# Kernel tuning notes

Measured on AMD Instinct MI355X. Metric: run time of the kernel, lower is better.

Reference implementation:

```python
import jax, jax.numpy as jnp
import numpy as np

VALUE_RANGE = 16
D_MODEL = 1024
NUM_TILES = 8
NUM_FREQS = 6
BATCH = 65536
TEMPERATURE = 0.5


def _fourier(x):
    # x: (B,) -> (B, 2*NUM_FREQS); freqs = 2**[0..F)
    freqs = 2.0 ** jnp.arange(NUM_FREQS, dtype=jnp.float32)
    ang = x[:, None] * (2.0 * np.pi / VALUE_RANGE) * freqs[None, :]
    return jnp.concatenate([jnp.sin(ang), jnp.cos(ang)], axis=-1)


def _layernorm(x, g, b, eps=1e-5):
    m = jnp.mean(x, axis=-1, keepdims=True)
    v = jnp.var(x, axis=-1, keepdims=True)
    return (x - m) * jax.lax.rsqrt(v + eps) * g + b


def _gelu(x):
    return jax.nn.gelu(x, approximate=False)  # torch nn.GELU() default is exact erf


def setup_inputs() -> dict:
    key = jax.random.key(0)
    ks = jax.random.split(key, 16)
    d, T, F4 = D_MODEL, NUM_TILES, 4 * NUM_FREQS
    s = lambda i, shape, scale: (jax.random.normal(ks[i], shape, jnp.float32) * scale)
    return {
        "a": jax.random.uniform(ks[0], (BATCH,), jnp.float32, 0.0, float(VALUE_RANGE)),
        "b": jax.random.uniform(ks[1], (BATCH,), jnp.float32, 0.0, float(VALUE_RANGE)),
        "W_in": s(2, (F4, d), 0.05), "b_in": jnp.zeros((d,), jnp.float32),
        "ln_g": jnp.ones((d,), jnp.float32), "ln_b": jnp.zeros((d,), jnp.float32),
        "Wr1_sum": s(3, (d, d), 0.03), "br1_sum": jnp.zeros((d,), jnp.float32),
        "Wr2_sum": s(4, (d, T), 0.03), "br2_sum": jnp.zeros((T,), jnp.float32),
        "Wr1_diff": s(5, (d, d), 0.03), "br1_diff": jnp.zeros((d,), jnp.float32),
        "Wr2_diff": s(6, (d, T), 0.03), "br2_diff": jnp.zeros((T,), jnp.float32),
        "We1": s(7, (T, d, 2 * d), 0.03), "be1": jnp.zeros((T, 2 * d), jnp.float32),
        "We2": s(8, (T, 2 * d, d), 0.02), "be2": jnp.zeros((T, d), jnp.float32),
        "w_sum": s(9, (d,), 0.03), "bs": jnp.zeros((), jnp.float32),
        "w_diff": s(10, (d,), 0.03), "bd": jnp.zeros((), jnp.float32),
    }


def reference(a, b, W_in, b_in, ln_g, ln_b,
              Wr1_sum, br1_sum, Wr2_sum, br2_sum,
              Wr1_diff, br1_diff, Wr2_diff, br2_diff,
              We1, be1, We2, be2, w_sum, bs, w_diff, bd):
    # Shared encoder
    x = jnp.concatenate([_fourier(a), _fourier(b)], axis=-1)      # (B, 4F)
    x = _gelu(_layernorm(x @ W_in + b_in, ln_g, ln_b))            # (B, d)
    # Top-1 routing (temperature scaling does not change argmax, kept for fidelity)
    sum_logits = (_gelu(x @ Wr1_sum + br1_sum) @ Wr2_sum + br2_sum) / TEMPERATURE
    diff_logits = (_gelu(x @ Wr1_diff + br1_diff) @ Wr2_diff + br2_diff) / TEMPERATURE
    sum_tile = jnp.argmax(sum_logits, axis=-1)                    # (B,)
    diff_tile = jnp.argmax(diff_logits, axis=-1)                  # (B,)
    # Expert dispatch: loop over small fixed num_tiles, mask-combine per token.
    sum_hidden = jnp.zeros_like(x)
    diff_hidden = jnp.zeros_like(x)
    for t in range(We1.shape[0]):
        y = _gelu(x @ We1[t] + be1[t]) @ We2[t] + be2[t]          # (B, d)
        sum_hidden = sum_hidden + jnp.where((sum_tile == t)[:, None], y, 0.0)
        diff_hidden = diff_hidden + jnp.where((diff_tile == t)[:, None], y, 0.0)
    sum_pred = sum_hidden @ w_sum + bs                            # (B,)
    diff_pred = diff_hidden @ w_diff + bd                         # (B,)
    return (sum_pred, diff_pred)
```

## Files before the change

### kernel.cpp

```cpp
#include <hip/hip_runtime.h>
#include <math.h>


#define BT 65536
#define QN 65536
#define TSTR QN
#define D 1024
#define NT 8
#define DH 2048
#define RCAP 8192
#define RTOK 8
#define DELTA 0.010f
#define XJCAP 768

typedef _Float16 f16;
typedef _Float16 f16x8 __attribute__((ext_vector_type(8)));
typedef _Float16 f16x4 __attribute__((ext_vector_type(4)));
typedef float f32x16 __attribute__((ext_vector_type(16)));

__device__ __forceinline__ float gelu_f(float v) {
    return 0.5f * v * (1.0f + erff(v * 0.70710678118654752440f));
}

__device__ __forceinline__ float gelu_fast(float x) {
    float ax = fabsf(x) * 0.70710678118654752440f;
    float t = __builtin_amdgcn_rcpf(1.0f + 0.3275911f * ax);
    float p = t * (0.254829592f + t * (-0.284496736f + t * (1.421413741f +
              t * (-1.453152027f + t * 1.061405429f))));
    float er = 1.0f - p * __expf(-ax * ax);
    er = copysignf(er, x);
    return 0.5f * x * (1.0f + er);
}

__device__ __forceinline__ void gload16(const void* g, void* l) {
    __builtin_amdgcn_global_load_lds(
        (const __attribute__((address_space(1))) void*)g,
        (__attribute__((address_space(3))) void*)l, 16, 0, 0);
}

__global__ __launch_bounds__(256) void k_prev(
    const float* __restrict__ We2, const float* __restrict__ w_sum,
    const float* __restrict__ w_diff, const float* __restrict__ be2,
    const float* __restrict__ bs, const float* __restrict__ bd,
    float* __restrict__ v_sum, float* __restrict__ v_diff,
    float* __restrict__ c_sum, float* __restrict__ c_diff)
{
    int bid = blockIdx.x;
    if (bid < 4096) {
        int row  = bid * 4 + (threadIdx.x >> 6);
        int lane = threadIdx.x & 63;
        const float* r = We2 + (size_t)row * D;
        float s1 = 0.f, s2 = 0.f;
        #pragma unroll
        for (int i = 0; i < 4; i++) {
            int o4 = (lane + 64 * i) * 4;
            float4 w = *(const float4*)(r + o4);
            float4 u = *(const float4*)(w_sum + o4);
            float4 v = *(const float4*)(w_diff + o4);
            s1 += w.x*u.x + w.y*u.y + w.z*u.z + w.w*u.w;
            s2 += w.x*v.x + w.y*v.y + w.z*v.z + w.w*v.w;
        }
        #pragma unroll
        for (int m = 32; m >= 1; m >>= 1) {
            s1 += __shfl_xor(s1, m, 64);
            s2 += __shfl_xor(s2, m, 64);
        }
        if (lane == 0) { v_sum[row] = s1; v_diff[row] = s2; }
    } else {
        int t = threadIdx.x;
        if (t < 8) {
            float s = 0.f; const float* r = be2 + t * D;
            for (int k = 0; k < D; k++) s += r[k] * w_sum[k];
            c_sum[t] = s + bs[0];
        } else if (t < 16) {
            int tt = t - 8;
            float s = 0.f; const float* r = be2 + tt * D;
            for (int k = 0; k < D; k++) s += r[k] * w_diff[k];
            c_diff[tt] = s + bd[0];
        }
    }
}

__global__ __launch_bounds__(256) void k_cvt(
    const float* __restrict__ We1, f16* __restrict__ We1T)
{
    __shared__ float tile[64][65];
    int b = blockIdx.x;
    int e = b >> 9, rem = b & 511;
    int kt = rem >> 5, nt = rem & 31;
    int tid = threadIdx.x;
    const float* src = We1 + ((size_t)e * D + kt * 64) * DH + nt * 64;
    #pragma unroll
    for (int i = 0; i < 16; i++) {
        int idx = tid + 256 * i;
        int kk = idx >> 6, nn = idx & 63;
        tile[kk][nn] = src[(size_t)kk * DH + nn];
    }
    __syncthreads();
    f16* dst = We1T + ((size_t)e * DH + nt * 64) * D + kt * 64;
    #pragma unroll
    for (int i = 0; i < 16; i++) {
        int idx = tid + 256 * i;
        int nn = idx >> 6, kk = idx & 63;
        dst[(size_t)nn * D + kk] = (f16)tile[kk][nn];
    }
}

__global__ __launch_bounds__(256) void k_cvtR(
    const float* __restrict__ Wr1s, const float* __restrict__ Wr1d,
    f16* __restrict__ Wr1Tf)
{
    __shared__ float tile[64][65];
    int b = blockIdx.x;
    int z = b >> 8, rem = b & 255;
    int kt = rem >> 4, nt2 = rem & 15;
    int tid = threadIdx.x;
    const float* W = z ? Wr1d : Wr1s;
    const float* src = W + (size_t)(kt * 64) * 1024 + nt2 * 64;
    #pragma unroll
    for (int i = 0; i < 16; i++) {
        int idx = tid + 256 * i;
        int kk = idx >> 6, nn = idx & 63;
        tile[kk][nn] = src[(size_t)kk * 1024 + nn];
    }
    __syncthreads();
    f16* dst = Wr1Tf + (size_t)(z * 1024 + nt2 * 64) * 1024 + kt * 64;
    #pragma unroll
    for (int i = 0; i < 16; i++) {
        int idx = tid + 256 * i;
        int nn = idx >> 6, kk = idx & 63;
        dst[(size_t)nn * 1024 + kk] = (f16)tile[kk][nn];
    }
}

__global__ __launch_bounds__(256) void k_fuse(
    const float* __restrict__ br1s, const float* __restrict__ br1d,
    const float* __restrict__ Wr2s, const float* __restrict__ Wr2d,
    float* __restrict__ br1f, float* __restrict__ w2f)
{
    int tid = threadIdx.x;
    for (int n = tid; n < 2048; n += 256) {
        br1f[n] = (n < 1024) ? br1s[n] : br1d[n - 1024];
        const float* src = (n < 1024) ? (Wr2s + (size_t)n * 8)
                                      : (Wr2d + (size_t)(n - 1024) * 8);
        #pragma unroll
        for (int o = 0; o < 8; o++) w2f[(size_t)n * 8 + o] = src[o];
    }
}

__global__ __launch_bounds__(256) void k_enc(
    const float* __restrict__ a, const float* __restrict__ b,
    const float* __restrict__ W_in, const float* __restrict__ b_in,
    const float* __restrict__ ln_g, const float* __restrict__ ln_b,
    f16* __restrict__ xh)
{
    __shared__ float x0[64][24];
    __shared__ float red[8];
    int tid = threadIdx.x;
    float4 Wc[24];
    #pragma unroll
    for (int f = 0; f < 24; f++) Wc[f] = *(const float4*)(W_in + f * D + tid * 4);
    float4 bi = *(const float4*)(b_in + tid * 4);
    float4 gg = *(const float4*)(ln_g + tid * 4);
    float4 bb = *(const float4*)(ln_b + tid * 4);
    int base = blockIdx.x * 64;

    for (int idx = tid; idx < 64 * 12; idx += 256) {
        int t = idx / 12, q = idx - t * 12;
        int fr = q % 6;
        float in = (q < 6) ? a[base + t] : b[base + t];
        float ang = (in * 0.39269908169872414f) * (float)(1 << fr);
        int off = (q < 6) ? 0 : 12;
        x0[t][off + fr]     = sinf(ang);
        x0[t][off + 6 + fr] = cosf(ang);
    }
    __syncthreads();

    int lane = tid & 63, wid = tid >> 6;
    for (int t = 0; t < 64; t++) {
        float4 p = bi;
        #pragma unroll
        for (int f = 0; f < 24; f++) {
            float xv = x0[t][f];
            p.x += xv * Wc[f].x; p.y += xv * Wc[f].y;
            p.z += xv * Wc[f].z; p.w += xv * Wc[f].w;
        }
        float s1 = p.x + p.y + p.z + p.w;
        float s2 = p.x*p.x + p.y*p.y + p.z*p.z + p.w*p.w;
        #pragma unroll
        for (int m = 32; m >= 1; m >>= 1) {
            s1 += __shfl_xor(s1, m, 64);
            s2 += __shfl_xor(s2, m, 64);
        }
        if (lane == 0) { red[wid] = s1; red[4 + wid] = s2; }
        __syncthreads();
        float mean = (red[0] + red[1] + red[2] + red[3]) * (1.f / 1024.f);
        float ms   = (red[4] + red[5] + red[6] + red[7]) * (1.f / 1024.f);
        float inv  = 1.f / sqrtf(ms - mean * mean + 1e-5f);
        float4 o;
        o.x = gelu_f((p.x - mean) * inv * gg.x + bb.x);
        o.y = gelu_f((p.y - mean) * inv * gg.y + bb.y);
        o.z = gelu_f((p.z - mean) * inv * gg.z + bb.z);
        o.w = gelu_f((p.w - mean) * inv * gg.w + bb.w);
        size_t row = (size_t)(blockIdx.x * 64 + t);
        f16x4 h; h[0] = (f16)o.x; h[1] = (f16)o.y; h[2] = (f16)o.z; h[3] = (f16)o.w;
        *(f16x4*)(xh + row * D + tid * 4) = h;
        __syncthreads();
    }
}

__global__ __launch_bounds__(256, 3) void k_rtrm(
    const f16* __restrict__ xh, const f16* __restrict__ Wr1Tf,
    const float* __restrict__ br1f, const float* __restrict__ w2f,
    float* __restrict__ part)
{
    __shared__ char smem[40960] __attribute__((aligned(16)));
    int bid = blockIdx.x;
    int ntile = bid & 7;
    int ttile = bid >> 3;
    int tid = threadIdx.x;
    int lane = tid & 63, wid = tid >> 6;
    int hi = lane >> 5, l31 = lane & 31;
    int sg = tid >> 3, sc = tid & 7;

    const char* xb = (const char*)xh + (size_t)(ttile * 64) * 2048;
    const char* wb = (const char*)Wr1Tf + (size_t)(ntile * 256) * 2048;
    size_t goff = (size_t)sg * 2048 + (size_t)((sc * 16) ^ ((sg & 7) << 4));

    int axor = (l31 & 7) << 4;
    int kx[4];
    #pragma unroll
    for (int ks = 0; ks < 4; ks++) kx[ks] = (ks * 32 + hi * 16) ^ axor;
    int arow[2], brow[2];
    #pragma unroll
    for (int mi = 0; mi < 2; mi++) arow[mi] = (wid * 64 + mi * 32 + l31) * 128;
    #pragma unroll
    for (int ni = 0; ni < 2; ni++) brow[ni] = 32768 + (ni * 32 + l31) * 128;

    f32x16 acc[2][2];
    #pragma unroll
    for (int mi = 0; mi < 2; mi++)
        #pragma unroll
        for (int ni = 0; ni < 2; ni++) acc[mi][ni] = (f32x16)(0.0f);

    for (int k0 = 0; k0 < 1024; k0 += 64) {
        __syncthreads();
        #pragma unroll
        for (int i = 0; i < 8; i++)
            gload16(wb + (size_t)i * 32 * 2048 + k0 * 2 + goff,
                    smem + i * 4096 + wid * 1024);
        #pragma unroll
        for (int i = 0; i < 2; i++)
            gload16(xb + (size_t)i * 32 * 2048 + k0 * 2 + goff,
                    smem + 32768 + i * 4096 + wid * 1024);
        __syncthreads();
        #pragma unroll
        for (int ks = 0; ks < 4; ks++) {
            f16x8 a0 = *(const f16x8*)(smem + arow[0] + kx[ks]);
            f16x8 a1 = *(const f16x8*)(smem + arow[1] + kx[ks]);
            f16x8 b0 = *(const f16x8*)(smem + brow[0] + kx[ks]);
            f16x8 b1 = *(const f16x8*)(smem + brow[1] + kx[ks]);
            acc[0][0] = __builtin_amdgcn_mfma_f32_32x32x16_f16(a0, b0, acc[0][0], 0, 0, 0);
            acc[0][1] = __builtin_amdgcn_mfma_f32_32x32x16_f16(a0, b1, acc[0][1], 0, 0, 0);
            acc[1][0] = __builtin_amdgcn_mfma_f32_32x32x16_f16(a1, b0, acc[1][0], 0, 0, 0);
            acc[1][1] = __builtin_amdgcn_mfma_f32_32x32x16_f16(a1, b1, acc[1][1], 0, 0, 0);
        }
    }

    float lp[2][8] = {};
    #pragma unroll
    for (int mi = 0; mi < 2; mi++) {
        #pragma unroll
        for (int r = 0; r < 16; r++) {
            int nl = wid * 64 + mi * 32 + (r & 3) + 8 * (r >> 2) + 4 * hi;
            int gn = ntile * 256 + nl;
            float b1 = br1f[gn];
            float4 wa = *(const float4*)(w2f + (size_t)gn * 8);
            float4 wc = *(const float4*)(w2f + (size_t)gn * 8 + 4);
            float h0 = gelu_fast(acc[mi][0][r] + b1);
            float h1 = gelu_fast(acc[mi][1][r] + b1);
            lp[0][0] += h0*wa.x; lp[0][1] += h0*wa.y;
            lp[0][2] += h0*wa.z; lp[0][3] += h0*wa.w;
            lp[0][4] += h0*wc.x; lp[0][5] += h0*wc.y;
            lp[0][6] += h0*wc.z; lp[0][7] += h0*wc.w;
            lp[1][0] += h1*wa.x; lp[1][1] += h1*wa.y;
            lp[1][2] += h1*wa.z; lp[1][3] += h1*wa.w;
            lp[1][4] += h1*wc.x; lp[1][5] += h1*wc.y;
            lp[1][6] += h1*wc.z; lp[1][7] += h1*wc.w;
        }
    }
    #pragma unroll
    for (int ni = 0; ni < 2; ni++)
        #pragma unroll
        for (int o = 0; o < 8; o++)
            lp[ni][o] += __shfl_xor(lp[ni][o], 32, 64);
    __syncthreads();
    float* redf = (float*)smem;
    if (hi == 0) {
        #pragma unroll
        for (int ni = 0; ni < 2; ni++)
            #pragma unroll
            for (int o = 0; o < 8; o++)
                redf[(wid * 64 + ni * 32 + l31) * 8 + o] = lp[ni][o];
    }
    __syncthreads();
    for (int idx = tid; idx < 512; idx += 256) {
        int tok = idx >> 3, o = idx & 7;
        float s = ((redf[(0 * 64 + tok) * 8 + o]  + redf[(1 * 64 + tok) * 8 + o])
                 +  redf[(2 * 64 + tok) * 8 + o]) + redf[(3 * 64 + tok) * 8 + o];
        part[((size_t)(ttile * 64 + tok) * 8 + ntile) * 8 + o] = s;
    }
}

__device__ __forceinline__ void emit_tasks(int tok, int ts, int td,
                                           int* tasks, int* cnts)
{
    if (ts == td) {
        int s = atomicAdd(&cnts[ts], 1);
        tasks[ts * TSTR + s] = tok | (3 << 17);
    } else {
        int s1 = atomicAdd(&cnts[ts], 1);
        tasks[ts * TSTR + s1] = tok | (1 << 17);
        int s2 = atomicAdd(&cnts[td], 1);
        tasks[td * TSTR + s2] = tok | (2 << 17);
    }
}

__global__ __launch_bounds__(256) void k_amx2(
    const float* __restrict__ part, const float* __restrict__ b2s,
    const float* __restrict__ b2d, int* __restrict__ tasks,
    int* __restrict__ ctrl, int* __restrict__ redoS, int* __restrict__ redoD)
{
    int i = blockIdx.x * 256 + threadIdx.x;
    const float* p = part + (size_t)i * 64;
    float Ls[8], Ld[8];
    #pragma unroll
    for (int o = 0; o < 8; o++) { Ls[o] = b2s[o]; Ld[o] = b2d[o]; }
    #pragma unroll
    for (int nt = 0; nt < 4; nt++)
        #pragma unroll
        for (int o = 0; o < 8; o++) Ls[o] += p[nt * 8 + o];
    #pragma unroll
    for (int nt = 4; nt < 8; nt++)
        #pragma unroll
        for (int o = 0; o < 8; o++) Ld[o] += p[nt * 8 + o];

    int as = 0; float m1s = Ls[0];
    #pragma unroll
    for (int o = 1; o < 8; o++) if (Ls[o] > m1s) { m1s = Ls[o]; as = o; }
    float m2s = -1e30f;
    #pragma unroll
    for (int o = 0; o < 8; o++) if (o != as && Ls[o] > m2s) m2s = Ls[o];
    int ad = 0; float m1d = Ld[0];
    #pragma unroll
    for (int o = 1; o < 8; o++) if (Ld[o] > m1d) { m1d = Ld[o]; ad = o; }
    float m2d = -1e30f;
    #pragma unroll
    for (int o = 0; o < 8; o++) if (o != ad && Ld[o] > m2d) m2d = Ld[o];

    bool sM = (m1s - m2s) < DELTA;
    bool dM = (m1d - m2d) < DELTA;
    if (!sM && !dM) { emit_tasks(i, as, ad, tasks, ctrl); return; }
    int posS = -1, posD = -1;
    if (sM) { posS = atomicAdd(&ctrl[8], 1); if (posS >= RCAP) { sM = false; posS = -1; } }
    if (dM) { posD = atomicAdd(&ctrl[9], 1); if (posD >= RCAP) { dM = false; posD = -1; } }
    if (!sM && !dM) { emit_tasks(i, as, ad, tasks, ctrl); return; }
    if (sM) redoS[posS] = i | (ad << 17) | ((dM ? 1 : 0) << 20);
    if (dM) redoD[posD] = i | (as << 17) | ((sM ? 1 : 0) << 20);
}

__global__ __launch_bounds__(256) void k_redo(
    const float* __restrict__ a, const float* __restrict__ b,
    const float* __restrict__ W_in, const float* __restrict__ b_in,
    const float* __restrict__ ln_g, const float* __restrict__ ln_b,
    const float* __restrict__ Wr1s, const float* __restrict__ br1s,
    const float* __restrict__ Wr2s,
    const float* __restrict__ Wr1d, const float* __restrict__ br1d,
    const float* __restrict__ Wr2d,
    const int* __restrict__ redoS, const int* __restrict__ redoD,
    const int* __restrict__ ctrl,
    float* __restrict__ rlogpS, float* __restrict__ rlogpD)
{
    int z = blockIdx.y;
    int rcnt = min(ctrl[8 + z], RCAP);
    int s0 = blockIdx.x * RTOK;
    if (s0 >= rcnt) return;
    const int* list = z ? redoD : redoS;
    const float* Wr1 = z ? Wr1d : Wr1s;
    const float* br1v = z ? br1d : br1s;
    const float* Wr2 = z ? Wr2d : Wr2s;

    __shared__ float xl[RTOK][1024];
    __shared__ float x0[RTOK][24];
    __shared__ float wred[4][RTOK][2];
    __shared__ float lred[4][RTOK][8];
    __shared__ int tokR[RTOK];
    int tid = threadIdx.x;
    int lane = tid & 63, wid = tid >> 6;

    if (tid < RTOK) tokR[tid] = list[min(s0 + tid, rcnt - 1)] & 0xFFFF;
    __syncthreads();

    if (tid < RTOK * 12) {
        int t = tid / 12, q = tid - t * 12;
        int fr = q % 6;
        int tok = tokR[t];
        float in = (q < 6) ? a[tok] : b[tok];
        float ang = (in * 0.39269908169872414f) * (float)(1 << fr);
        int off = (q < 6) ? 0 : 12;
        x0[t][off + fr]     = sinf(ang);
        x0[t][off + 6 + fr] = cosf(ang);
    }
    __syncthreads();

    {
        float4 Wc[24];
        #pragma unroll
        for (int f = 0; f < 24; f++) Wc[f] = *(const float4*)(W_in + f * D + tid * 4);
        float4 bi = *(const float4*)(b_in + tid * 4);
        float4 gg = *(const float4*)(ln_g + tid * 4);
        float4 bb = *(const float4*)(ln_b + tid * 4);
        float p[RTOK][4];
        #pragma unroll
        for (int r = 0; r < RTOK; r++) {
            float4 pv = bi;
            #pragma unroll
            for (int f = 0; f < 24; f++) {
                float xv = x0[r][f];
                pv.x += xv * Wc[f].x; pv.y += xv * Wc[f].y;
                pv.z += xv * Wc[f].z; pv.w += xv * Wc[f].w;
            }
            p[r][0] = pv.x; p[r][1] = pv.y; p[r][2] = pv.z; p[r][3] = pv.w;
            float s1 = pv.x + pv.y + pv.z + pv.w;
            float s2 = pv.x*pv.x + pv.y*pv.y + pv.z*pv.z + pv.w*pv.w;
            #pragma unroll
            for (int m = 32; m >= 1; m >>= 1) {
                s1 += __shfl_xor(s1, m, 64);
                s2 += __shfl_xor(s2, m, 64);
            }
            if (lane == 0) { wred[wid][r][0] = s1; wred[wid][r][1] = s2; }
        }
        __syncthreads();
        #pragma unroll
        for (int r = 0; r < RTOK; r++) {
            float mean = (wred[0][r][0] + wred[1][r][0] + wred[2][r][0] + wred[3][r][0]) * (1.f / 1024.f);
            float ms   = (wred[0][r][1] + wred[1][r][1] + wred[2][r][1] + wred[3][r][1]) * (1.f / 1024.f);
            float inv  = 1.f / sqrtf(ms - mean * mean + 1e-5f);
            float gv[4] = {gg.x, gg.y, gg.z, gg.w};
            float bv[4] = {bb.x, bb.y, bb.z, bb.w};
            #pragma unroll
            for (int jj = 0; jj < 4; jj++)
                xl[r][tid * 4 + jj] = gelu_f((p[r][jj] - mean) * inv * gv[jj] + bv[jj]);
        }
    }
    __syncthreads();

    int c0 = tid * 4;
    float hacc[RTOK][4] = {};
    #pragma unroll 4
    for (int k = 0; k < 1024; k++) {
        float4 wv = *(const float4*)(Wr1 + (size_t)k * 1024 + c0);
        #pragma unroll
        for (int r = 0; r < RTOK; r++) {
            float xv = xl[r][k];
            hacc[r][0] += xv * wv.x; hacc[r][1] += xv * wv.y;
            hacc[r][2] += xv * wv.z; hacc[r][3] += xv * wv.w;
        }
    }
    float L[RTOK][8] = {};
    #pragma unroll
    for (int jj = 0; jj < 4; jj++) {
        int col = c0 + jj;
        float b1 = br1v[col];
        float4 wa = *(const float4*)(Wr2 + (size_t)col * 8);
        float4 wc = *(const float4*)(Wr2 + (size_t)col * 8 + 4);
        #pragma unroll
        for (int r = 0; r < RTOK; r++) {
            float h = gelu_f(hacc[r][jj] + b1);
            L[r][0] += h*wa.x; L[r][1] += h*wa.y; L[r][2] += h*wa.z; L[r][3] += h*wa.w;
            L[r][4] += h*wc.x; L[r][5] += h*wc.y; L[r][6] += h*wc.z; L[r][7] += h*wc.w;
        }
    }
    #pragma unroll
    for (int m = 32; m >= 1; m >>= 1)
        #pragma unroll
        for (int r = 0; r < RTOK; r++)
            #pragma unroll
            for (int o = 0; o < 8; o++)
                L[r][o] += __shfl_xor(L[r][o], m, 64);
    if (lane == 0) {
        #pragma unroll
        for (int r = 0; r < RTOK; r++)
            #pragma unroll
            for (int o = 0; o < 8; o++)
                lred[wid][r][o] = L[r][o];
    }
    __syncthreads();
    if (tid < RTOK * 8) {
        int r = tid >> 3, o = tid & 7;
        int slot = s0 + r;
        if (slot < rcnt) {
            float v = ((lred[0][r][o] + lred[1][r][o]) + lred[2][r][o]) + lred[3][r][o];
            float* dst = z ? rlogpD : rlogpS;
            dst[(size_t)slot * 8 + o] = v;
        }
    }
}

__global__ __launch_bounds__(256) void k_amx3d(
    const float* __restrict__ rlogpD, const int* __restrict__ redoD,
    const float* __restrict__ b2d, int* __restrict__ tasks,
    int* __restrict__ ctrl, int* __restrict__ adx)
{
    int rcnt = min(ctrl[9], RCAP);
    for (int s = blockIdx.x * 256 + threadIdx.x; s < rcnt; s += gridDim.x * 256) {
        int entry = redoD[s];
        int tok = entry & 0xFFFF;
        float L[8];
        #pragma unroll
        for (int o = 0; o < 8; o++) L[o] = rlogpD[(size_t)s * 8 + o] + b2d[o];
        int td = 0; float bv = L[0];
        #pragma unroll
        for (int o = 1; o < 8; o++) if (L[o] > bv) { bv = L[o]; td = o; }
        adx[tok] = td;
        if (!((entry >> 20) & 1))
            emit_tasks(tok, (entry >> 17) & 7, td, tasks, ctrl);
    }
}

__global__ __launch_bounds__(256) void k_amx3s(
    const float* __restrict__ rlogpS, const int* __restrict__ redoS,
    const float* __restrict__ b2s, int* __restrict__ tasks,
    int* __restrict__ ctrl, const int* __restrict__ adx)
{
    int rcnt = min(ctrl[8], RCAP);
    for (int s = blockIdx.x * 256 + threadIdx.x; s < rcnt; s += gridDim.x * 256) {
        int entry = redoS[s];
        int tok = entry & 0xFFFF;
        float L[8];
        #pragma unroll
        for (int o = 0; o < 8; o++) L[o] = rlogpS[(size_t)s * 8 + o] + b2s[o];
        int ts = 0; float bv = L[0];
        #pragma unroll
        for (int o = 1; o < 8; o++) if (L[o] > bv) { bv = L[o]; ts = o; }
        int td = ((entry >> 20) & 1) ? adx[tok] : ((entry >> 17) & 7);
        emit_tasks(tok, ts, td, tasks, ctrl);
    }
}

__global__ void k_sched(const int* __restrict__ ctrl, int* __restrict__ xjob)
{
    __shared__ int seg[17];
    __shared__ int Jt[2];
    int tid = threadIdx.x;
    if (tid == 0) {
        int o = 0;
        for (int e = 0; e < 8; e++) {
            int nt2 = (ctrl[e] + 127) >> 7;
            seg[e * 2]     = o; o += nt2;
            seg[e * 2 + 1] = o; o += nt2;
        }
        seg[16] = o;
        Jt[0] = o; Jt[1] = (o + 7) >> 3;
    }
    __syncthreads();
    int J = Jt[0], target = Jt[1];
    for (int g = tid; g < J; g += blockDim.x) {
        int s = 0;
        while (s < 15 && seg[s + 1] <= g) s++;
        int e = s >> 1, ch = s & 1, rt = g - seg[s];
        int x = g / target; if (x > 7) x = 7;
        int pos = g - x * target;
        xjob[x * XJCAP + pos] = e | (ch << 3) | (rt << 4);
    }
    if (tid < 8) {
        int c = J - tid * target;
        if (c < 0) c = 0;
        if (c > target) c = target;
        xjob[8 * XJCAP + tid] = c;
    }
}

__global__ __launch_bounds__(256) void k_expm(
    const f16* __restrict__ xh, const f16* __restrict__ We1T,
    const float* __restrict__ be1, const float* __restrict__ v_sum,
    const float* __restrict__ v_diff, const float* __restrict__ c_sum,
    const float* __restrict__ c_diff, const int* __restrict__ tasks,
    const int* __restrict__ counts, const int* __restrict__ xjob,
    float* __restrict__ ppS, float* __restrict__ ppD)
{
    int xcd  = blockIdx.x & 7;
    int slot = blockIdx.x >> 3;
    int nj = xjob[8 * XJCAP + xcd];

    __shared__ char smem[65536] __attribute__((aligned(16)));
    __shared__ int tokL[128];
    __shared__ int flgL[128];
    __shared__ float redS[2][128];
    __shared__ float redD[2][128];

    int tid = threadIdx.x;
    int lane = tid & 63;
    int wid  = tid >> 6;
    int wr = wid >> 1, wc = wid & 1;
    int hi = lane >> 5, l31 = lane & 31;
    int sg = tid >> 3, sc = tid & 7;
    int goffc = (sc * 16) ^ ((sg & 7) << 4);

    const char* xh_b = (const char*)xh;

    int axor = (l31 & 7) << 4;
    int kx[4];
    #pragma unroll
    for (int ks = 0; ks < 4; ks++) kx[ks] = (ks * 32 + hi * 16) ^ axor;
    int arow[2], brow[2];
    #pragma unroll
    for (int mi = 0; mi < 2; mi++) arow[mi] = (wr * 64 + mi * 32 + l31) * 128;
    #pragma unroll
    for (int ni = 0; ni < 2; ni++) brow[ni] = 16384 + (wc * 64 + ni * 32 + l31) * 128;

    for (int j = slot; j < nj; j += 256) {
        int jv = xjob[xcd * XJCAP + j];
        int e  = jv & 7;
        int ch = (jv >> 3) & 1;
        int rt = jv >> 4;
        int cnt = counts[e];
        int r0 = rt * 128;
        const char* bbase = (const char*)(We1T + (size_t)e * DH * D);

        __syncthreads();
        if (tid < 128) {
            int idx = r0 + tid;
            int tv = tasks[e * TSTR + min(idx, cnt - 1)];
            tokL[tid] = tv & 0xFFFF;
            flgL[tid] = (idx < cnt) ? ((tv >> 17) & 3) : 0;
        }
        __syncthreads();
        size_t asrc[4];
        #pragma unroll
        for (int i = 0; i < 4; i++)
            asrc[i] = (size_t)tokL[i * 32 + sg] * 2048 + goffc;

        float ss[2][16] = {}, sd[2][16] = {};
        f32x16 acc[2][2];
        #pragma unroll
        for (int mi = 0; mi < 2; mi++)
            #pragma unroll
            for (int ni = 0; ni < 2; ni++) acc[mi][ni] = (f32x16)(0.0f);

        auto STAGE = [&](int p, int bb) {
            int n0 = ch * 1024 + (p >> 4) * 128;
            int k0b = (p & 15) * 128;
            char* ldsA = smem + bb * 32768 + wid * 1024;
            char* ldsB = smem + bb * 32768 + 16384 + wid * 1024;
            #pragma unroll
            for (int i = 0; i < 4; i++)
                gload16(xh_b + asrc[i] + k0b, ldsA + i * 4096);
            const char* bs = bbase + ((size_t)n0 + sg) * 2048 + k0b + goffc;
            #pragma unroll
            for (int i = 0; i < 4; i++)
                gload16(bs + (size_t)i * 32 * 2048, ldsB + i * 4096);
        };

        STAGE(0, 0);
        __syncthreads();
        for (int p = 0; p < 128; ++p) {
            int bb = p & 1;
            if (p < 127) STAGE(p + 1, bb ^ 1);
            const char* base = smem + bb * 32768;
            #pragma unroll
            for (int ks = 0; ks < 4; ks++) {
                f16x8 a0 = *(const f16x8*)(base + arow[0] + kx[ks]);
                f16x8 a1 = *(const f16x8*)(base + arow[1] + kx[ks]);
                f16x8 b0 = *(const f16x8*)(base + brow[0] + kx[ks]);
                f16x8 b1 = *(const f16x8*)(base + brow[1] + kx[ks]);
                acc[0][0] = __builtin_amdgcn_mfma_f32_32x32x16_f16(a0, b0, acc[0][0], 0, 0, 0);
                acc[0][1] = __builtin_amdgcn_mfma_f32_32x32x16_f16(a0, b1, acc[0][1], 0, 0, 0);
                acc[1][0] = __builtin_amdgcn_mfma_f32_32x32x16_f16(a1, b0, acc[1][0], 0, 0, 0);
                acc[1][1] = __builtin_amdgcn_mfma_f32_32x32x16_f16(a1, b1, acc[1][1], 0, 0, 0);
            }
            if ((p & 15) == 15) {
                int n0 = ch * 1024 + (p >> 4) * 128;
                #pragma unroll
                for (int ni = 0; ni < 2; ni++) {
                    int col = n0 + wc * 64 + ni * 32 + l31;
                    float b1 = be1[e * DH + col];
                    float vs = v_sum[(size_t)e * DH + col];
                    float vd = v_diff[(size_t)e * DH + col];
                    #pragma unroll
                    for (int mi = 0; mi < 2; mi++) {
                        #pragma unroll
                        for (int r = 0; r < 16; r++) {
                            float h = gelu_fast(acc[mi][ni][r] + b1);
                            ss[mi][r] += h * vs;
                            sd[mi][r] += h * vd;
                        }
                    }
                }
                #pragma unroll
                for (int mi = 0; mi < 2; mi++)
                    #pragma unroll
                    for (int ni = 0; ni < 2; ni++) acc[mi][ni] = (f32x16)(0.0f);
            }
            __syncthreads();
        }

        #pragma unroll
        for (int m = 16; m >= 1; m >>= 1) {
            #pragma unroll
            for (int mi = 0; mi < 2; mi++)
                #pragma unroll
                for (int r = 0; r < 16; r++) {
                    ss[mi][r] += __shfl_xor(ss[mi][r], m, 64);
                    sd[mi][r] += __shfl_xor(sd[mi][r], m, 64);
                }
        }
        if (l31 == 0) {
            #pragma unroll
            for (int mi = 0; mi < 2; mi++)
                #pragma unroll
                for (int r = 0; r < 16; r++) {
                    int row = wr * 64 + mi * 32 + (r & 3) + 8 * (r >> 2) + 4 * hi;
                    redS[wc][row] = ss[mi][r];
                    redD[wc][row] = sd[mi][r];
                }
        }
        __syncthreads();
        if (tid < 128) {
            int idx = r0 + tid;
            if (idx < cnt) {
                int fl = flgL[tid];
                int tok = tokL[tid];
                float s = redS[0][tid] + redS[1][tid];
                float d = redD[0][tid] + redD[1][tid];
                if (ch == 0) { s += c_sum[e]; d += c_diff[e]; }
                if (fl & 1) ppS[ch * QN + tok] = s;
                if (fl & 2) ppD[ch * QN + tok] = d;
            }
        }
    }
}

__global__ __launch_bounds__(256) void k_fin(
    const float* __restrict__ ppS, const float* __restrict__ ppD,
    float* __restrict__ out)
{
    int i = blockIdx.x * 256 + threadIdx.x;
    out[i]      = ppS[i] + ppS[QN + i];
    out[BT + i] = ppD[i] + ppD[QN + i];
}

extern "C" void kernel_launch(void* const* d_in, const int* in_sizes, int n_in,
                              void* d_out, int out_size, void* d_ws, size_t ws_size,
                              hipStream_t stream)
{
    const float* a      = (const float*)d_in[0];
    const float* b      = (const float*)d_in[1];
    const float* W_in   = (const float*)d_in[2];
    const float* b_in   = (const float*)d_in[3];
    const float* ln_g   = (const float*)d_in[4];
    const float* ln_b   = (const float*)d_in[5];
    const float* Wr1s   = (const float*)d_in[6];
    const float* br1s   = (const float*)d_in[7];
    const float* Wr2s   = (const float*)d_in[8];
    const float* br2s   = (const float*)d_in[9];
    const float* Wr1d   = (const float*)d_in[10];
    const float* br1d   = (const float*)d_in[11];
    const float* Wr2d   = (const float*)d_in[12];
    const float* br2d   = (const float*)d_in[13];
    const float* We1    = (const float*)d_in[14];
    const float* be1    = (const float*)d_in[15];
    const float* We2    = (const float*)d_in[16];
    const float* be2    = (const float*)d_in[17];
    const float* w_sum  = (const float*)d_in[18];
    const float* bs     = (const float*)d_in[19];
    const float* w_diff = (const float*)d_in[20];
    const float* bd     = (const float*)d_in[21];
    float* out = (float*)d_out;

    char* w = (char*)d_ws;
    size_t off = 0;
    auto alloc = [&](size_t bytes) -> char* {
        char* p = w + off;
        off = (off + bytes + 255) & ~(size_t)255;
        return p;
    };
    float* v_sum   = (float*)alloc((size_t)NT * DH * 4);
    float* v_diff  = (float*)alloc((size_t)NT * DH * 4);
    float* c_sum   = (float*)alloc(64);
    float* c_diff  = (float*)alloc(64);
    f16*   xh      = (f16*)alloc((size_t)QN * D * 2);
    float* part    = (float*)alloc((size_t)QN * 64 * 4);
    float* rlogpS  = (float*)alloc((size_t)RCAP * 8 * 4);
    float* rlogpD  = (float*)alloc((size_t)RCAP * 8 * 4);
    int*   redoS   = (int*)alloc((size_t)RCAP * 4);
    int*   redoD   = (int*)alloc((size_t)RCAP * 4);
    int*   adx     = (int*)alloc((size_t)QN * 4);
    int*   tasks   = (int*)alloc((size_t)NT * QN * 4);
    int*   ctrl    = (int*)alloc(64);
    int*   xjob    = (int*)alloc((size_t)(8 * XJCAP + 8) * 4);
    float* ppS     = (float*)alloc((size_t)2 * QN * 4);
    float* ppD     = (float*)alloc((size_t)2 * QN * 4);
    f16*   We1T    = (f16*)alloc((size_t)NT * DH * D * 2);
    f16*   Wr1Tf   = (f16*)alloc((size_t)2048 * 1024 * 2);
    float* br1f    = (float*)alloc((size_t)2048 * 4);
    float* w2f     = (float*)alloc((size_t)2048 * 8 * 4);
    if (off > ws_size) {
        hipMemsetAsync(d_out, 0, (size_t)out_size * 4, stream);
        return;
    }

    k_cvt <<<dim3(4096), dim3(256), 0, stream>>>(We1, We1T);
    k_cvtR<<<dim3(512),  dim3(256), 0, stream>>>(Wr1s, Wr1d, Wr1Tf);
    k_fuse<<<dim3(1),    dim3(256), 0, stream>>>(br1s, br1d, Wr2s, Wr2d, br1f, w2f);
    k_prev<<<dim3(4097), dim3(256), 0, stream>>>(We2, w_sum, w_diff, be2, bs, bd,
                                                 v_sum, v_diff, c_sum, c_diff);
    k_enc<<<dim3(QN / 64), dim3(256), 0, stream>>>(a, b, W_in, b_in, ln_g, ln_b, xh);
    k_rtrm<<<dim3(QN / 64 * 8), dim3(256), 0, stream>>>(xh, Wr1Tf, br1f, w2f, part);
    hipMemsetAsync(ctrl, 0, 64, stream);
    k_amx2<<<dim3(QN / 256), dim3(256), 0, stream>>>(part, br2s, br2d, tasks, ctrl,
                                                     redoS, redoD);
    k_redo<<<dim3(RCAP / RTOK, 2), dim3(256), 0, stream>>>(
        a, b, W_in, b_in, ln_g, ln_b,
        Wr1s, br1s, Wr2s, Wr1d, br1d, Wr2d,
        redoS, redoD, ctrl, rlogpS, rlogpD);
    k_amx3d<<<dim3(16), dim3(256), 0, stream>>>(rlogpD, redoD, br2d, tasks, ctrl, adx);
    k_amx3s<<<dim3(16), dim3(256), 0, stream>>>(rlogpS, redoS, br2s, tasks, ctrl, adx);
    k_sched<<<dim3(1), dim3(256), 0, stream>>>(ctrl, xjob);
    k_expm<<<dim3(2048), dim3(256), 0, stream>>>(xh, We1T, be1, v_sum, v_diff,
                                                 c_sum, c_diff, tasks, ctrl, xjob,
                                                 ppS, ppD);
    k_fin<<<dim3(QN / 256), dim3(256), 0, stream>>>(ppS, ppD, out);
}
```

Measured before the change: 3.041 ms.

## Widen expert GEMM N-tile to 256 and triple-buffer LDS with explicit waitcnts

The expert first-layer MFMA kernel now computes a 128x256 output tile per block, with each wave holding 2x4 accumulators instead of 2x2. Each A fragment is therefore reused across twice as many B columns. The LDS pipeline grows from double to triple buffering (144KB of shared memory), using manual s_waitcnt vmcnt counts and raw s_barrier so two stages of global loads stay in flight. The trade-off is lower occupancy, since only one block fits per CU, plus higher accumulator register pressure.

```diff
diff --git a/kernel.cpp b/kernel.cpp
--- a/kernel.cpp
+++ b/kernel.cpp
@@ -593,7 +593,7 @@
     int slot = blockIdx.x >> 3;
     int nj = xjob[8 * XJCAP + xcd];
 
-    __shared__ char smem[65536] __attribute__((aligned(16)));
+    __shared__ char smem[147456] __attribute__((aligned(16)));
     __shared__ int tokL[128];
     __shared__ int flgL[128];
     __shared__ float redS[2][128];
@@ -613,11 +613,11 @@
     int kx[4];
     #pragma unroll
     for (int ks = 0; ks < 4; ks++) kx[ks] = (ks * 32 + hi * 16) ^ axor;
-    int arow[2], brow[2];
+    int arow[2], nrow[4];
     #pragma unroll
     for (int mi = 0; mi < 2; mi++) arow[mi] = (wr * 64 + mi * 32 + l31) * 128;
     #pragma unroll
-    for (int ni = 0; ni < 2; ni++) brow[ni] = 16384 + (wc * 64 + ni * 32 + l31) * 128;
+    for (int ni = 0; ni < 4; ni++) nrow[ni] = 16384 + (wc * 128 + ni * 32 + l31) * 128;
 
     for (int j = slot; j < nj; j += 256) {
         int jv = xjob[xcd * XJCAP + j];
@@ -642,48 +642,53 @@
             asrc[i] = (size_t)tokL[i * 32 + sg] * 2048 + goffc;
 
         float ss[2][16] = {}, sd[2][16] = {};
-        f32x16 acc[2][2];
+        f32x16 acc[2][4];
         #pragma unroll
         for (int mi = 0; mi < 2; mi++)
             #pragma unroll
-            for (int ni = 0; ni < 2; ni++) acc[mi][ni] = (f32x16)(0.0f);
+            for (int ni = 0; ni < 4; ni++) acc[mi][ni] = (f32x16)(0.0f);
 
         auto STAGE = [&](int p, int bb) {
-            int n0 = ch * 1024 + (p >> 4) * 128;
+            int n0 = ch * 1024 + (p >> 4) * 256;
             int k0b = (p & 15) * 128;
-            char* ldsA = smem + bb * 32768 + wid * 1024;
-            char* ldsB = smem + bb * 32768 + 16384 + wid * 1024;
+            char* bufb = smem + bb * 49152;
             #pragma unroll
             for (int i = 0; i < 4; i++)
-                gload16(xh_b + asrc[i] + k0b, ldsA + i * 4096);
+                gload16(xh_b + asrc[i] + k0b, bufb + i * 4096 + wid * 1024);
             const char* bs = bbase + ((size_t)n0 + sg) * 2048 + k0b + goffc;
             #pragma unroll
-            for (int i = 0; i < 4; i++)
-                gload16(bs + (size_t)i * 32 * 2048, ldsB + i * 4096);
+            for (int i = 0; i < 8; i++)
+                gload16(bs + (size_t)i * 32 * 2048,
+                        bufb + 16384 + i * 4096 + wid * 1024);
         };
 
         STAGE(0, 0);
-        __syncthreads();
-        for (int p = 0; p < 128; ++p) {
-            int bb = p & 1;
-            if (p < 127) STAGE(p + 1, bb ^ 1);
-            const char* base = smem + bb * 32768;
+        STAGE(1, 1);
+        for (int p = 0; p < 64; ++p) {
+            int bb = p % 3;
+            if (p + 2 < 64) STAGE(p + 2, (p + 2) % 3);
+            if (p + 2 < 64)      asm volatile("s_waitcnt vmcnt(24)");
+            else if (p + 1 < 64) asm volatile("s_waitcnt vmcnt(12)");
+            else                 asm volatile("s_waitcnt vmcnt(0)");
+            __builtin_amdgcn_s_barrier();
+            __builtin_amdgcn_sched_barrier(0);
+            const char* base = smem + bb * 49152;
             #pragma unroll
             for (int ks = 0; ks < 4; ks++) {
                 f16x8 a0 = *(const f16x8*)(base + arow[0] + kx[ks]);
                 f16x8 a1 = *(const f16x8*)(base + arow[1] + kx[ks]);
-                f16x8 b0 = *(const f16x8*)(base + brow[0] + kx[ks]);
-                f16x8 b1 = *(const f16x8*)(base + brow[1] + kx[ks]);
-                acc[0][0] = __builtin_amdgcn_mfma_f32_32x32x16_f16(a0, b0, acc[0][0], 0, 0, 0);
-                acc[0][1] = __builtin_amdgcn_mfma_f32_32x32x16_f16(a0, b1, acc[0][1], 0, 0, 0);
-                acc[1][0] = __builtin_amdgcn_mfma_f32_32x32x16_f16(a1, b0, acc[1][0], 0, 0, 0);
-                acc[1][1] = __builtin_amdgcn_mfma_f32_32x32x16_f16(a1, b1, acc[1][1], 0, 0, 0);
+                #pragma unroll
+                for (int ni = 0; ni < 4; ni++) {
+                    f16x8 bf = *(const f16x8*)(base + nrow[ni] + kx[ks]);
+                    acc[0][ni] = __builtin_amdgcn_mfma_f32_32x32x16_f16(a0, bf, acc[0][ni], 0, 0, 0);
+                    acc[1][ni] = __builtin_amdgcn_mfma_f32_32x32x16_f16(a1, bf, acc[1][ni], 0, 0, 0);
+                }
             }
             if ((p & 15) == 15) {
-                int n0 = ch * 1024 + (p >> 4) * 128;
+                int n0 = ch * 1024 + (p >> 4) * 256;
                 #pragma unroll
-                for (int ni = 0; ni < 2; ni++) {
-                    int col = n0 + wc * 64 + ni * 32 + l31;
+                for (int ni = 0; ni < 4; ni++) {
+                    int col = n0 + wc * 128 + ni * 32 + l31;
                     float b1 = be1[e * DH + col];
                     float vs = v_sum[(size_t)e * DH + col];
                     float vd = v_diff[(size_t)e * DH + col];
@@ -700,9 +705,10 @@
                 #pragma unroll
                 for (int mi = 0; mi < 2; mi++)
                     #pragma unroll
-                    for (int ni = 0; ni < 2; ni++) acc[mi][ni] = (f32x16)(0.0f);
+                    for (int ni = 0; ni < 4; ni++) acc[mi][ni] = (f32x16)(0.0f);
             }
-            __syncthreads();
+            __builtin_amdgcn_s_barrier();
+            __builtin_amdgcn_sched_barrier(0);
         }
 
         #pragma unroll
```

New measurement: 2.772 ms. 1.1x faster.
